# Performance work log

Measured on AMD Instinct MI355X. Metric: run time of the kernel, lower is better.

## Reference

```python
import jax, jax.numpy as jnp
import numpy as np

N, E, IN, HID, OUT, K = 10000, 320000, 256, 256, 128, 3


def setup_inputs() -> dict:
    key = jax.random.key(0)
    ks = jax.random.split(key, 4)
    x = jax.random.normal(ks[0], (N, IN), jnp.float32)
    edge = jax.random.randint(ks[1], (2, E), 0, N)

    def glorot(k, shape):
        lim = (6.0 / (shape[-2] + shape[-1])) ** 0.5
        return jax.random.uniform(k, shape, jnp.float32, -lim, lim)

    W1 = glorot(ks[2], (K, IN, HID))
    b1 = jnp.zeros((HID,), jnp.float32)
    W2 = glorot(ks[3], (K, HID, OUT))
    b2 = jnp.zeros((OUT,), jnp.float32)
    return {"x": x, "edge": edge, "W1": W1, "b1": b1, "W2": W2, "b2": b2}


def _cheb_conv(x, src, dst, norm, W, b):
    # Chebyshev recursion: Tx_0 = x, Tx_1 = L_hat x, Tx_k = 2 L_hat Tx_{k-1} - Tx_{k-2}
    n = x.shape[0]

    def prop(t):  # sparse L_hat @ t via edge gather/scatter
        return jax.ops.segment_sum(t[src] * norm[:, None], dst, num_segments=n)

    Tx0 = x
    out = jnp.einsum('ni,io->no', Tx0, W[0])
    Tx1 = prop(Tx0)
    out = out + jnp.einsum('ni,io->no', Tx1, W[1])
    for k in range(2, W.shape[0]):
        Tx2 = 2.0 * prop(Tx1) - Tx0
        out = out + jnp.einsum('ni,io->no', Tx2, W[k])
        Tx0, Tx1 = Tx1, Tx2
    return out + b


def reference(x, edge, W1, b1, W2, b2):
    src, dst = edge[0], edge[1]
    # symmetric normalization, lambda_max = 2.0 (PyG ChebConv default):
    # L_hat = 2/lambda_max * (I - D^-1/2 A D^-1/2) - I = -D^-1/2 A D^-1/2 (zero diagonal)
    deg = jax.ops.segment_sum(jnp.ones((src.shape[0],), jnp.float32), dst, num_segments=x.shape[0])
    dis = jnp.where(deg > 0, jax.lax.rsqrt(jnp.maximum(deg, 1.0)), 0.0)
    norm = -dis[src] * dis[dst]  # [E]
    h = jax.nn.relu(_cheb_conv(x, src, dst, norm, W1, b1))
    # dropout is identity in eval mode
    return _cheb_conv(h, src, dst, norm, W2, b2)
```

## Files before the change

kernel.cpp:

```cpp
#include <hip/hip_runtime.h>


constexpr int N   = 10000;
constexpr int E   = 320000;
constexpr int KS  = 8;
constexpr int MT  = 626;
constexpr int CAP = 96;

using bf16x8 = __attribute__((ext_vector_type(8))) short;
using f32x4  = __attribute__((ext_vector_type(4))) float;

__device__ inline float b2f(ushort u) { return __uint_as_float((unsigned)u << 16); }
__device__ inline ushort f2b(float f) {
    unsigned u = __float_as_uint(f);
    unsigned r = (u + 0x7fffu + ((u >> 16) & 1u)) >> 16;
    return (ushort)r;
}
__device__ inline size_t pidx(int r, int c) {
    return (size_t)((r >> 4) * KS + (c >> 5)) * 512 + ((c & 31) >> 3) * 128 + (r & 15) * 8 + (c & 7);
}

__global__ void conv_all(const float* __restrict__ x,
                         const float* __restrict__ W1, const float* __restrict__ W2,
                         ushort* __restrict__ PA1, ushort* __restrict__ PA2,
                         ushort* __restrict__ PB1, ushort* __restrict__ PB2,
                         int* __restrict__ cnt) {
    int t = blockIdx.x * blockDim.x + threadIdx.x;
    if (t < N * 32) {
        if (t < 16384) cnt[t] = 0;
        int n = t >> 5, f = (t & 31) * 8;
        float4 v0 = *reinterpret_cast<const float4*>(x + (size_t)n * 256 + f);
        float4 v1 = *reinterpret_cast<const float4*>(x + (size_t)n * 256 + f + 4);
        bf16x8 o;
        o[0] = (short)f2b(v0.x); o[1] = (short)f2b(v0.y); o[2] = (short)f2b(v0.z); o[3] = (short)f2b(v0.w);
        o[4] = (short)f2b(v1.x); o[5] = (short)f2b(v1.y); o[6] = (short)f2b(v1.z); o[7] = (short)f2b(v1.w);
        *reinterpret_cast<bf16x8*>(PA1 + pidx(n, f)) = o;
        return;
    }
    t -= N * 32;
    if (t < 768 * 256) {
        int o = t % 768, i = t / 768;
        float val;
        if (o < 256)      val = W1[2 * 65536 + i * 256 + o];
        else if (o < 512) val = W1[1 * 65536 + i * 256 + (o - 256)];
        else              val = W1[i * 256 + (o - 512)] - W1[2 * 65536 + i * 256 + (o - 512)];
        PB1[pidx(o, i)] = f2b(val);
        return;
    }
    t -= 768 * 256;
    if (t < 384 * 256) {
        int o = t % 384, i = t / 384;
        float val;
        if (o < 128)      val = W2[2 * 32768 + i * 128 + o];
        else if (o < 256) val = W2[1 * 32768 + i * 128 + (o - 128)];
        else              val = W2[i * 128 + (o - 256)] - W2[2 * 32768 + i * 128 + (o - 256)];
        PB2[pidx(o, i)] = f2b(val);
        return;
    }
    t -= 384 * 256;
    if (t < 8192) {
        size_t pad = (size_t)625 * KS * 512;
        if (t < 4096) PA1[pad + t] = 0;
        else          PA2[pad + (t - 4096)] = 0;
    }
}

__global__ void scatter_kernel(const int* __restrict__ src, const int* __restrict__ dst,
                               int* __restrict__ cnt, int* __restrict__ bucket) {
    int e = blockIdx.x * blockDim.x + threadIdx.x;
    if (e >= E) return;
    int s = src[e], d = dst[e];
    int pos = atomicAdd(&cnt[d], 1);
    if (pos < CAP) bucket[(size_t)d * CAP + pos] = s;
}

template<bool L2OUT>
__global__ __launch_bounds__(256) void
mfma_gemm(const ushort* __restrict__ PA, const ushort* __restrict__ PB,
          ushort* __restrict__ out16, float* __restrict__ out32,
          const int* __restrict__ cntv, float* __restrict__ disv) {
    int tid = threadIdx.x, lane = tid & 63, wv = tid >> 6;
    if (cntv && blockIdx.y == 0) {
        int g = blockIdx.x * 256 + tid;
        if (g < N) { int c = cntv[g]; disv[g] = c > 0 ? rsqrtf((float)c) : 0.f; }
    }
    int mt0 = blockIdx.x * 2;
    int ot0 = (blockIdx.y * 4 + wv) * 6;
    const ushort* Abase = PA + (size_t)mt0 * (KS * 512) + lane * 8;
    const ushort* Bbase = PB + (size_t)ot0 * (KS * 512) + lane * 8;

    f32x4 acc[2][6] = {};
    bf16x8 aX[2], bX[6], aY[2], bY[6];

    auto LD = [&](int ks, bf16x8 (&a)[2], bf16x8 (&b)[6]) {
#pragma unroll
        for (int mi = 0; mi < 2; ++mi)
            a[mi] = *reinterpret_cast<const bf16x8*>(Abase + (size_t)mi * (KS * 512) + ks * 512);
#pragma unroll
        for (int ni = 0; ni < 6; ++ni)
            b[ni] = *reinterpret_cast<const bf16x8*>(Bbase + (size_t)ni * (KS * 512) + ks * 512);
    };
    auto CP = [&](bf16x8 (&a)[2], bf16x8 (&b)[6]) {
#pragma unroll
        for (int mi = 0; mi < 2; ++mi)
#pragma unroll
            for (int ni = 0; ni < 6; ++ni)
                acc[mi][ni] = __builtin_amdgcn_mfma_f32_16x16x32_bf16(a[mi], b[ni], acc[mi][ni], 0, 0, 0);
    };

    LD(0, aX, bX);
#pragma unroll
    for (int ks = 0; ks < KS; ++ks) {
        if (ks & 1) { if (ks + 1 < KS) LD(ks + 1, aX, bX); CP(aY, bY); }
        else        { if (ks + 1 < KS) LD(ks + 1, aY, bY); CP(aX, bX); }
    }

    int colBase = lane & 15;
    int rowBase = (lane >> 4) * 4;
#pragma unroll
    for (int mi = 0; mi < 2; ++mi)
#pragma unroll
        for (int ni = 0; ni < 6; ++ni) {
            int col = (ot0 + ni) * 16 + colBase;
#pragma unroll
            for (int j = 0; j < 4; ++j) {
                int row = (mt0 + mi) * 16 + rowBase + j;
                if (row < N) {
                    float v = acc[mi][ni][j];
                    if (!L2OUT) {
                        out16[(size_t)row * 768 + col] = f2b(v);
                    } else {
                        if (col < 256) out16[(size_t)row * 256 + col] = f2b(v);
                        else           out32[(size_t)row * 128 + (col - 256)] = v;
                    }
                }
            }
        }
}

template<int W, int MODE>
__global__ void prop(const int* __restrict__ cnt, const float* __restrict__ dis,
                     const int* __restrict__ bucket,
                     const ushort* __restrict__ tin, int tstride,
                     const ushort* __restrict__ lin16, int lstride,
                     const float* __restrict__ lin32, const float* __restrict__ bias,
                     ushort* __restrict__ out16, float* __restrict__ out32) {
    constexpr int LPN = W / 8;
    int tid = threadIdx.x;
    int d = blockIdx.x * (256 / LPN) + tid / LPN;
    int f = (tid % LPN) * 8;
    int nE = min(cnt[d], CAP);
    const int* bk = bucket + (size_t)d * CAP;
    float dd = dis[d];
    const ushort* tf = tin + f;
    float accA[8] = {}, accB[8] = {};
    int i = 0;
    for (; i + 4 <= nE; i += 4) {
        int4 s4 = *reinterpret_cast<const int4*>(bk + i);
        float w0 = dis[s4.x], w1 = dis[s4.y], w2 = dis[s4.z], w3 = dis[s4.w];
        bf16x8 v0 = *reinterpret_cast<const bf16x8*>(tf + (size_t)s4.x * tstride);
        bf16x8 v1 = *reinterpret_cast<const bf16x8*>(tf + (size_t)s4.y * tstride);
        bf16x8 v2 = *reinterpret_cast<const bf16x8*>(tf + (size_t)s4.z * tstride);
        bf16x8 v3 = *reinterpret_cast<const bf16x8*>(tf + (size_t)s4.w * tstride);
#pragma unroll
        for (int j = 0; j < 8; ++j) {
            accA[j] += b2f((ushort)v0[j]) * w0 + b2f((ushort)v2[j]) * w2;
            accB[j] += b2f((ushort)v1[j]) * w1 + b2f((ushort)v3[j]) * w3;
        }
    }
    for (; i < nE; ++i) {
        int s = bk[i];
        float w = dis[s];
        bf16x8 v0 = *reinterpret_cast<const bf16x8*>(tf + (size_t)s * tstride);
#pragma unroll
        for (int j = 0; j < 8; ++j) accA[j] += b2f((ushort)v0[j]) * w;
    }
#pragma unroll
    for (int j = 0; j < 8; ++j) accA[j] += accB[j];

    if (MODE == 0) {
        bf16x8 z = *reinterpret_cast<const bf16x8*>(lin16 + (size_t)d * lstride + f);
        bf16x8 o;
#pragma unroll
        for (int j = 0; j < 8; ++j) o[j] = (short)f2b(b2f((ushort)z[j]) - 2.f * dd * accA[j]);
        *reinterpret_cast<bf16x8*>(out16 + (size_t)d * W + f) = o;
    } else if (MODE == 1) {
        bf16x8 z = *reinterpret_cast<const bf16x8*>(lin16 + (size_t)d * lstride + f);
        bf16x8 o;
#pragma unroll
        for (int j = 0; j < 8; ++j)
            o[j] = (short)f2b(fmaxf(b2f((ushort)z[j]) + bias[f + j] - dd * accA[j], 0.f));
        *reinterpret_cast<bf16x8*>(out16 + pidx(d, f)) = o;
    } else {
        float4 z0 = *reinterpret_cast<const float4*>(lin32 + (size_t)d * W + f);
        float4 z1 = *reinterpret_cast<const float4*>(lin32 + (size_t)d * W + f + 4);
        float zz[8] = {z0.x, z0.y, z0.z, z0.w, z1.x, z1.y, z1.z, z1.w};
        float r[8];
#pragma unroll
        for (int j = 0; j < 8; ++j) r[j] = zz[j] + bias[f + j] - dd * accA[j];
        *reinterpret_cast<float4*>(out32 + (size_t)d * W + f)     = make_float4(r[0], r[1], r[2], r[3]);
        *reinterpret_cast<float4*>(out32 + (size_t)d * W + f + 4) = make_float4(r[4], r[5], r[6], r[7]);
    }
}

extern "C" void kernel_launch(void* const* d_in, const int* in_sizes, int n_in,
                              void* d_out, int out_size, void* d_ws, size_t ws_size,
                              hipStream_t stream) {
    const float* x  = (const float*)d_in[0];
    const int* edge = (const int*)d_in[1];
    const float* W1 = (const float*)d_in[2];
    const float* b1 = (const float*)d_in[3];
    const float* W2 = (const float*)d_in[4];
    const float* b2 = (const float*)d_in[5];
    const int* src = edge;
    const int* dst = edge + E;
    float* out = (float*)d_out;

    int*    cnt    = (int*)d_ws;
    float*  dis    = (float*)(cnt + 16384);
    int*    bucket = (int*)(dis + 16384);
    ushort* PA1 = (ushort*)(bucket + (size_t)N * CAP);
    ushort* PA2 = PA1 + (size_t)MT * KS * 512;
    ushort* PB1 = PA2 + (size_t)MT * KS * 512;
    ushort* PB2 = PB1 + (size_t)48 * KS * 512;
    ushort* Z1  = PB2 + (size_t)24 * KS * 512;
    ushort* V1  = Z1 + (size_t)N * 768;
    ushort* Zb  = V1 + (size_t)N * 256;
    ushort* V2  = Zb + (size_t)N * 256;
    float*  Z0f = (float*)(V2 + (size_t)N * 128);

    constexpr int CONV_T = N * 32 + 768 * 256 + 384 * 256 + 8192;

    conv_all<<<(CONV_T + 255) / 256, 256, 0, stream>>>(x, W1, W2, PA1, PA2, PB1, PB2, cnt);
    scatter_kernel<<<(E + 255) / 256, 256, 0, stream>>>(src, dst, cnt, bucket);

    mfma_gemm<false><<<dim3(MT / 2, 2), 256, 0, stream>>>(PA1, PB1, Z1, nullptr, cnt, dis);
    prop<256, 0><<<N / 8, 256, 0, stream>>>(cnt, dis, bucket,
                                            Z1, 768, Z1 + 256, 768, nullptr, nullptr, V1, nullptr);
    prop<256, 1><<<N / 8, 256, 0, stream>>>(cnt, dis, bucket,
                                            V1, 256, Z1 + 512, 768, nullptr, b1, PA2, nullptr);
    mfma_gemm<true><<<dim3(MT / 2, 1), 256, 0, stream>>>(PA2, PB2, Zb, Z0f, nullptr, nullptr);
    prop<128, 0><<<N / 16, 256, 0, stream>>>(cnt, dis, bucket,
                                             Zb, 256, Zb + 128, 256, nullptr, nullptr, V2, nullptr);
    prop<128, 2><<<N / 16, 256, 0, stream>>>(cnt, dis, bucket,
                                             V2, 128, nullptr, 0, Z0f, b2, nullptr, out);
}
```

Measured before the change: 120.5 us.

## Fuse edge bucketing into first GEMM launch and compute degree norms inline

Merges the edge scatter/bucketing kernel and the first MFMA GEMM into one launch, with separate block ranges for GEMM tiles and edge atomics, so the two independent jobs run concurrently. The precomputed dis array goes away: prop kernels compute rsqrt of the degree count on the fly for each neighbor. This removes one launch and a serialization point, at the cost of extra rsqrt and count gathers in the propagation inner loops and possible contention between GEMM and atomic blocks.

```diff
diff --git a/kernel.cpp b/kernel.cpp
--- a/kernel.cpp
+++ b/kernel.cpp
@@ -1,11 +1,11 @@
 #include <hip/hip_runtime.h>
 
 
-constexpr int N   = 10000;
-constexpr int E   = 320000;
-constexpr int KS  = 8;
-constexpr int MT  = 626;
-constexpr int CAP = 96;
+constexpr int N    = 10000;
+constexpr int E    = 320000;
+constexpr int KS   = 8;
+constexpr int MT   = 626;
+constexpr int CAP  = 96;
 
 using bf16x8 = __attribute__((ext_vector_type(8))) short;
 using f32x4  = __attribute__((ext_vector_type(4))) float;
@@ -19,6 +19,7 @@
 __device__ inline size_t pidx(int r, int c) {
     return (size_t)((r >> 4) * KS + (c >> 5)) * 512 + ((c & 31) >> 3) * 128 + (r & 15) * 8 + (c & 7);
 }
+__device__ inline float irs(int c) { return c > 0 ? rsqrtf((float)c) : 0.f; }
 
 __global__ void conv_all(const float* __restrict__ x,
                          const float* __restrict__ W1, const float* __restrict__ W2,
@@ -65,27 +66,10 @@
     }
 }
 
-__global__ void scatter_kernel(const int* __restrict__ src, const int* __restrict__ dst,
-                               int* __restrict__ cnt, int* __restrict__ bucket) {
-    int e = blockIdx.x * blockDim.x + threadIdx.x;
-    if (e >= E) return;
-    int s = src[e], d = dst[e];
-    int pos = atomicAdd(&cnt[d], 1);
-    if (pos < CAP) bucket[(size_t)d * CAP + pos] = s;
-}
-
 template<bool L2OUT>
-__global__ __launch_bounds__(256) void
-mfma_gemm(const ushort* __restrict__ PA, const ushort* __restrict__ PB,
-          ushort* __restrict__ out16, float* __restrict__ out32,
-          const int* __restrict__ cntv, float* __restrict__ disv) {
-    int tid = threadIdx.x, lane = tid & 63, wv = tid >> 6;
-    if (cntv && blockIdx.y == 0) {
-        int g = blockIdx.x * 256 + tid;
-        if (g < N) { int c = cntv[g]; disv[g] = c > 0 ? rsqrtf((float)c) : 0.f; }
-    }
-    int mt0 = blockIdx.x * 2;
-    int ot0 = (blockIdx.y * 4 + wv) * 6;
+__device__ void gemm_unit(int mt0, int ot0, int lane,
+                          const ushort* __restrict__ PA, const ushort* __restrict__ PB,
+                          ushort* __restrict__ out16, float* __restrict__ out32) {
     const ushort* Abase = PA + (size_t)mt0 * (KS * 512) + lane * 8;
     const ushort* Bbase = PB + (size_t)ot0 * (KS * 512) + lane * 8;
 
@@ -138,9 +122,33 @@
         }
 }
 
+__global__ __launch_bounds__(256) void
+sg1_kernel(const int* __restrict__ src, const int* __restrict__ dst,
+           int* __restrict__ cnt, int* __restrict__ bucket,
+           const ushort* __restrict__ PA, const ushort* __restrict__ PB,
+           ushort* __restrict__ Z1) {
+    int bid = blockIdx.x, tid = threadIdx.x;
+    if (bid < 626) {
+        int lane = tid & 63, wv = tid >> 6;
+        int mpair = bid >> 1, half = bid & 1;
+        gemm_unit<false>(mpair * 2, half * 24 + wv * 6, lane, PA, PB, Z1, nullptr);
+    } else {
+        int e = (bid - 626) * 256 + tid;
+        int s = src[e], d = dst[e];
+        int pos = atomicAdd(&cnt[d], 1);
+        if (pos < CAP) bucket[(size_t)d * CAP + pos] = s;
+    }
+}
+
+__global__ __launch_bounds__(256) void
+gemm2_kernel(const ushort* __restrict__ PA, const ushort* __restrict__ PB,
+             ushort* __restrict__ Zb, float* __restrict__ Z0f) {
+    int tid = threadIdx.x, lane = tid & 63, wv = tid >> 6;
+    gemm_unit<true>(blockIdx.x * 2, wv * 6, lane, PA, PB, Zb, Z0f);
+}
+
 template<int W, int MODE>
-__global__ void prop(const int* __restrict__ cnt, const float* __restrict__ dis,
-                     const int* __restrict__ bucket,
+__global__ void prop(const int* __restrict__ cnt, const int* __restrict__ bucket,
                      const ushort* __restrict__ tin, int tstride,
                      const ushort* __restrict__ lin16, int lstride,
                      const float* __restrict__ lin32, const float* __restrict__ bias,
@@ -149,15 +157,16 @@
     int tid = threadIdx.x;
     int d = blockIdx.x * (256 / LPN) + tid / LPN;
     int f = (tid % LPN) * 8;
-    int nE = min(cnt[d], CAP);
+    int cd = cnt[d];
+    int nE = min(cd, CAP);
+    float dd = irs(cd);
     const int* bk = bucket + (size_t)d * CAP;
-    float dd = dis[d];
     const ushort* tf = tin + f;
     float accA[8] = {}, accB[8] = {};
     int i = 0;
     for (; i + 4 <= nE; i += 4) {
         int4 s4 = *reinterpret_cast<const int4*>(bk + i);
-        float w0 = dis[s4.x], w1 = dis[s4.y], w2 = dis[s4.z], w3 = dis[s4.w];
+        float w0 = irs(cnt[s4.x]), w1 = irs(cnt[s4.y]), w2 = irs(cnt[s4.z]), w3 = irs(cnt[s4.w]);
         bf16x8 v0 = *reinterpret_cast<const bf16x8*>(tf + (size_t)s4.x * tstride);
         bf16x8 v1 = *reinterpret_cast<const bf16x8*>(tf + (size_t)s4.y * tstride);
         bf16x8 v2 = *reinterpret_cast<const bf16x8*>(tf + (size_t)s4.z * tstride);
@@ -170,7 +179,7 @@
     }
     for (; i < nE; ++i) {
         int s = bk[i];
-        float w = dis[s];
+        float w = irs(cnt[s]);
         bf16x8 v0 = *reinterpret_cast<const bf16x8*>(tf + (size_t)s * tstride);
 #pragma unroll
         for (int j = 0; j < 8; ++j) accA[j] += b2f((ushort)v0[j]) * w;
@@ -217,8 +226,7 @@
     float* out = (float*)d_out;
 
     int*    cnt    = (int*)d_ws;
-    float*  dis    = (float*)(cnt + 16384);
-    int*    bucket = (int*)(dis + 16384);
+    int*    bucket = cnt + 16384;
     ushort* PA1 = (ushort*)(bucket + (size_t)N * CAP);
     ushort* PA2 = PA1 + (size_t)MT * KS * 512;
     ushort* PB1 = PA2 + (size_t)MT * KS * 512;
@@ -232,16 +240,15 @@
     constexpr int CONV_T = N * 32 + 768 * 256 + 384 * 256 + 8192;
 
     conv_all<<<(CONV_T + 255) / 256, 256, 0, stream>>>(x, W1, W2, PA1, PA2, PB1, PB2, cnt);
-    scatter_kernel<<<(E + 255) / 256, 256, 0, stream>>>(src, dst, cnt, bucket);
-
-    mfma_gemm<false><<<dim3(MT / 2, 2), 256, 0, stream>>>(PA1, PB1, Z1, nullptr, cnt, dis);
-    prop<256, 0><<<N / 8, 256, 0, stream>>>(cnt, dis, bucket,
+    sg1_kernel<<<626 + 1250, 256, 0, stream>>>(src, dst, cnt, bucket, PA1, PB1, Z1);
+
+    prop<256, 0><<<N / 8, 256, 0, stream>>>(cnt, bucket,
                                             Z1, 768, Z1 + 256, 768, nullptr, nullptr, V1, nullptr);
-    prop<256, 1><<<N / 8, 256, 0, stream>>>(cnt, dis, bucket,
+    prop<256, 1><<<N / 8, 256, 0, stream>>>(cnt, bucket,
                                             V1, 256, Z1 + 512, 768, nullptr, b1, PA2, nullptr);
-    mfma_gemm<true><<<dim3(MT / 2, 1), 256, 0, stream>>>(PA2, PB2, Zb, Z0f, nullptr, nullptr);
-    prop<128, 0><<<N / 16, 256, 0, stream>>>(cnt, dis, bucket,
+    gemm2_kernel<<<313, 256, 0, stream>>>(PA2, PB2, Zb, Z0f);
+    prop<128, 0><<<N / 16, 256, 0, stream>>>(cnt, bucket,
                                              Zb, 256, Zb + 128, 256, nullptr, nullptr, V2, nullptr);
-    prop<128, 2><<<N / 16, 256, 0, stream>>>(cnt, dis, bucket,
+    prop<128, 2><<<N / 16, 256, 0, stream>>>(cnt, bucket,
                                              V2, 128, nullptr, 0, Z0f, b2, nullptr, out);
 }
```

Measured after the change: 115.0 us. 1.05x faster.
